# Performance work log

Hardware: AMD Instinct MI355X
Metric: run time of the kernel (lower is better)

Reference implementation:

```python
import jax, jax.numpy as jnp
import numpy as np

B, S, R, C_M = 1, 512, 256, 256   # batch, n_seq, n_res, msa channels
C_P, C_Z = 32, 128                # projection channels, pair channels


def setup_inputs() -> dict:
    key = jax.random.key(0)
    ks = jax.random.split(key, 8)
    M = jax.random.normal(ks[0], (B, S, R, C_M), dtype=jnp.float32)
    M_mask = jnp.ones((B, S, R), dtype=jnp.float32)
    Z_raw = jnp.zeros((B, R, R, C_Z), dtype=jnp.float32)
    # LayerNorm params
    ln_g = jnp.ones((C_M,), dtype=jnp.float32)
    ln_b = jnp.zeros((C_M,), dtype=jnp.float32)
    # linear_a / linear_b: glorot-uniform init
    lim = float(np.sqrt(6.0 / (C_M + C_P)))
    Wa = jax.random.uniform(ks[1], (C_P, C_M), minval=-lim, maxval=lim, dtype=jnp.float32)
    ba = jnp.zeros((C_P,), dtype=jnp.float32)
    Wb = jax.random.uniform(ks[2], (C_P, C_M), minval=-lim, maxval=lim, dtype=jnp.float32)
    bb = jnp.zeros((C_P,), dtype=jnp.float32)
    # o_linear is zero-initialized in the source; use small random weights so the
    # output is non-trivial for correctness testing (math is identical).
    Wo = jax.random.normal(ks[3], (C_Z, C_P * C_P), dtype=jnp.float32) * 0.02
    bo = jnp.zeros((C_Z,), dtype=jnp.float32)
    return {"M": M, "M_mask": M_mask, "Z_raw": Z_raw, "ln_g": ln_g, "ln_b": ln_b,
            "Wa": Wa, "ba": ba, "Wb": Wb, "bb": bb, "Wo": Wo, "bo": bo}


def _layernorm(x, g, b, eps=1e-5):
    mu = jnp.mean(x, axis=-1, keepdims=True)
    var = jnp.var(x, axis=-1, keepdims=True)
    return (x - mu) * jax.lax.rsqrt(var + eps) * g + b


def reference(M, M_mask, Z_raw, ln_g, ln_b, Wa, ba, Wb, bb, Wo, bo):
    Mn = _layernorm(M, ln_g, ln_b)                      # [b,s,i,c_m]
    mask = M_mask[..., None]                            # [b,s,i,1]
    left = (jnp.einsum('bsic,dc->bsid', Mn, Wa) + ba) * mask   # [b,s,i,d]
    right = (jnp.einsum('bsic,ec->bsie', Mn, Wb) + bb) * mask  # [b,s,j,e]
    # outer-product mean: contract over sequence dim s
    O = jnp.einsum('bsid,bsje->bijde', left, right)     # [b,i,j,d,e]
    b, i, j, d, e = O.shape
    O = O.reshape(b, i, j, d * e)
    Z = jnp.einsum('bijk,zk->bijz', O, Wo) + bo         # [b,i,j,c_z]
    norm = jnp.einsum('bsi,bsj->bij', M_mask, M_mask)[..., None]
    return Z / (1e-3 + norm)
```

## Files before the change

### kernel.cpp

```cpp
#include <hip/hip_runtime.h>
#include <hip/hip_bf16.h>
#include <stdint.h>

#define S_DIM 512
#define R_DIM 256
#define CM 256
#define CP 32
#define CZ 128

typedef __attribute__((ext_vector_type(8))) short bf16x8;
typedef __attribute__((ext_vector_type(4))) float f32x4;
typedef unsigned int u32;

__device__ __forceinline__ float bf2f(unsigned short u) {
  union { u32 i; float f; } v; v.i = ((u32)u) << 16; return v.f;
}
__device__ __forceinline__ unsigned short f2bf(float f) {
  union { float f; u32 i; } v; v.f = f;
  u32 x = v.i;
  u32 r = (x + 0x7FFFu + ((x >> 16) & 1u)) >> 16;
  return (unsigned short)r;
}

__device__ __forceinline__ void gload_lds16(const unsigned short* g, unsigned short* l) {
  __builtin_amdgcn_global_load_lds((const __attribute__((address_space(1))) u32*)(g),
                                   (__attribute__((address_space(3))) u32*)(l), 16, 0, 0);
}

__device__ __forceinline__ void wave_bar() {
  asm volatile("" ::: "memory");
  __builtin_amdgcn_s_barrier();
  asm volatile("" ::: "memory");
}

__global__ void prep_kernel(const float* __restrict__ Wa, const float* __restrict__ ba,
                            const float* __restrict__ Wb, const float* __restrict__ bb,
                            const float* __restrict__ ln_g, const float* __restrict__ ln_b,
                            unsigned short* __restrict__ wp, float* __restrict__ Ka,
                            float* __restrict__ Ca) {
  __shared__ float ska[4], sca[4];
  const int o = blockIdx.x;
  const int c = threadIdx.x;
  const float* W = (o < 32) ? (Wa + o * CM) : (Wb + (o - 32) * CM);
  float wv = W[c];
  unsigned short bv = f2bf(wv * ln_g[c]);
  wp[o * CM + c] = bv;
  float ka = bf2f(bv);
  float ca = wv * ln_b[c];
  #pragma unroll
  for (int m = 1; m < 64; m <<= 1) {
    ka += __shfl_xor(ka, m);
    ca += __shfl_xor(ca, m);
  }
  if ((c & 63) == 0) { ska[c >> 6] = ka; sca[c >> 6] = ca; }
  __syncthreads();
  if (c == 0) {
    Ka[o] = ska[0] + ska[1] + ska[2] + ska[3];
    Ca[o] = sca[0] + sca[1] + sca[2] + sca[3] + ((o < 32) ? ba[o] : bb[o - 32]);
  }
}

__global__ void cast_wo_kernel(const float* __restrict__ Wo, unsigned short* __restrict__ Wo_bf) {
  int idx = blockIdx.x * blockDim.x + threadIdx.x;
  if (idx < CZ * CP * CP) Wo_bf[idx] = f2bf(Wo[idx]);
}

__global__ void scale_kernel(const float* __restrict__ mask, float* __restrict__ scale) {
  int i = blockIdx.x, j = threadIdx.x;
  float sum = 0.f;
  for (int s = 0; s < S_DIM; ++s) {
    sum += mask[s * R_DIM + i] * mask[s * R_DIM + j];
  }
  scale[i * R_DIM + j] = 1.0f / (1e-3f + sum);
}

#define K1_ROWS 64
#define XPAD 264

__global__ __launch_bounds__(256) void
ln_proj_kernel(const float* __restrict__ M, const float* __restrict__ mask,
               const unsigned short* __restrict__ wp_g, const float* __restrict__ Ka_g,
               const float* __restrict__ Ca_g,
               unsigned short* __restrict__ leftT, unsigned short* __restrict__ rightT) {
  __shared__ unsigned short xt[K1_ROWS * XPAD];
  __shared__ unsigned short wp[64 * XPAD];
  __shared__ float smu[K1_ROWS], srs[K1_ROWS], smk[K1_ROWS];
  __shared__ float sKa[64], sCa[64];

  const int t = threadIdx.x;
  const int lane = t & 63;
  const int w = t >> 6;
  const int lm = lane & 15;
  const int rr = lane >> 4;
  const int i = blockIdx.x;
  const int s0 = blockIdx.y * K1_ROWS;

  for (int idx = t; idx < 64 * CM / 8; idx += 256) {
    int row = idx >> 5;
    int col = (idx & 31) * 8;
    *(uint4*)(&wp[row * XPAD + col]) = *(const uint4*)(wp_g + row * CM + col);
  }
  if (t < 64) { sKa[t] = Ka_g[t]; sCa[t] = Ca_g[t]; }

  #pragma unroll
  for (int it = 0; it < 4; ++it) {
    const int row = w * 16 + it * 4 + rr;
    const int sg = s0 + row;
    const float* src = M + ((size_t)sg * R_DIM + i) * CM;
    float4 x[4];
    #pragma unroll
    for (int ch = 0; ch < 4; ++ch) x[ch] = *(const float4*)(src + ch * 64 + lm * 4);
    float sum = 0.f, ssq = 0.f;
    #pragma unroll
    for (int ch = 0; ch < 4; ++ch) {
      sum += x[ch].x + x[ch].y + x[ch].z + x[ch].w;
      ssq += x[ch].x * x[ch].x + x[ch].y * x[ch].y + x[ch].z * x[ch].z + x[ch].w * x[ch].w;
    }
    #pragma unroll
    for (int m = 1; m < 16; m <<= 1) {
      sum += __shfl_xor(sum, m);
      ssq += __shfl_xor(ssq, m);
    }
    float mu = sum * (1.0f / CM);
    float var = ssq * (1.0f / CM) - mu * mu;
    float rs = rsqrtf(var + 1e-5f);
    if (lm == 0) {
      smu[row] = mu; srs[row] = rs;
      smk[row] = mask[(size_t)sg * R_DIM + i];
    }
    #pragma unroll
    for (int ch = 0; ch < 4; ++ch) {
      ushort4 xb;
      xb.x = f2bf(x[ch].x); xb.y = f2bf(x[ch].y); xb.z = f2bf(x[ch].z); xb.w = f2bf(x[ch].w);
      *(ushort4*)(&xt[row * XPAD + ch * 64 + lm * 4]) = xb;
    }
  }
  __syncthreads();

  f32x4 acc[4] = {{0.f, 0.f, 0.f, 0.f}, {0.f, 0.f, 0.f, 0.f},
                  {0.f, 0.f, 0.f, 0.f}, {0.f, 0.f, 0.f, 0.f}};
  #pragma unroll
  for (int k = 0; k < 8; ++k) {
    const int c0 = k * 32 + ((lane >> 4) << 3);
    bf16x8 a = *(const bf16x8*)(&wp[(w * 16 + (lane & 15)) * XPAD + c0]);
    #pragma unroll
    for (int nt = 0; nt < 4; ++nt) {
      bf16x8 b = *(const bf16x8*)(&xt[(nt * 16 + (lane & 15)) * XPAD + c0]);
      acc[nt] = __builtin_amdgcn_mfma_f32_16x16x32_bf16(a, b, acc[nt], 0, 0, 0);
    }
  }

  #pragma unroll
  for (int nt = 0; nt < 4; ++nt) {
    int srow = nt * 16 + (lane & 15);
    float mu = smu[srow], rs = srs[srow], mk = smk[srow];
    int sg = s0 + srow;
    #pragma unroll
    for (int r = 0; r < 4; ++r) {
      int o = w * 16 + ((lane >> 4) << 2) + r;
      float v = (rs * (acc[nt][r] - mu * sKa[o]) + sCa[o]) * mk;
      unsigned short bv = f2bf(v);
      if (o < 32) leftT[(size_t)(i * 32 + o) * S_DIM + sg] = bv;
      else        rightT[(size_t)(i * 32 + (o - 32)) * S_DIM + sg] = bv;
    }
  }
}

#define NT2 8

__global__ __launch_bounds__(512, 1) void
opm_gemm_kernel(const unsigned short* __restrict__ leftT, const unsigned short* __restrict__ rightT,
                const unsigned short* __restrict__ Wo_bf, const float* __restrict__ bo,
                const float* __restrict__ scale, float* __restrict__ out) {
  extern __shared__ unsigned short smem[];

  const int t = threadIdx.x;
  const int lane = t & 63;
  const int lm = lane & 15, lq = lane >> 4;
  const int sw = lm & 7;
  const int w = t >> 6;
  const int wm = w >> 2, wn = w & 3;

  const int bid = blockIdx.x;
  const int xcd = bid & 7, local = bid >> 3;
  const int by = xcd * 4 + (local & 3);
  const int bx = local >> 2;

  const unsigned short* Asrc = leftT + (size_t)(by * 256) * S_DIM;
  const unsigned short* Bsrc = rightT + (size_t)(bx * 256) * S_DIM;

  int sr[4], so[4];
  #pragma unroll
  for (int q = 0; q < 4; ++q) {
    int c = q * 512 + t;
    sr[q] = c >> 3;
    so[q] = ((c & 7) ^ ((c >> 3) & 7)) * 8;
  }

  f32x4 acc[8][4];
  #pragma unroll
  for (int a = 0; a < 8; ++a)
    #pragma unroll
    for (int b = 0; b < 4; ++b) acc[a][b] = (f32x4){0.f, 0.f, 0.f, 0.f};

  auto STAGE = [&](int kt, int buf) {
    const int kb = kt * 64;
    unsigned short* ab = smem + buf * 32768;
    #pragma unroll
    for (int q = 0; q < 4; ++q) {
      int c = q * 512 + t;
      gload_lds16(Asrc + (size_t)sr[q] * S_DIM + kb + so[q], ab + c * 8);
      gload_lds16(Bsrc + (size_t)sr[q] * S_DIM + kb + so[q], ab + 16384 + c * 8);
    }
  };

  STAGE(0, 0);
  STAGE(1, 1);

  #pragma unroll
  for (int kt = 0; kt < NT2; ++kt) {
    const int cur = kt & 1;
    if (kt < NT2 - 1) asm volatile("s_waitcnt vmcnt(8)" ::: "memory");
    else              asm volatile("s_waitcnt vmcnt(0)" ::: "memory");
    wave_bar();

    const unsigned short* Ab = smem + cur * 32768;
    const unsigned short* Bb = Ab + 16384;
    #pragma unroll
    for (int ks = 0; ks < 2; ++ks) {
      const int kp = ks * 4 + lq;
      const int slot = (kp ^ sw) << 3;
      bf16x8 af[8], bfr[4];
      #pragma unroll
      for (int mi = 0; mi < 8; ++mi)
        af[mi] = *(const bf16x8*)(&Ab[(wm * 128 + mi * 16 + lm) * 64 + slot]);
      #pragma unroll
      for (int ni = 0; ni < 4; ++ni)
        bfr[ni] = *(const bf16x8*)(&Bb[(wn * 64 + ni * 16 + lm) * 64 + slot]);
      #pragma unroll
      for (int mi = 0; mi < 8; ++mi)
        #pragma unroll
        for (int ni = 0; ni < 4; ++ni)
          acc[mi][ni] = __builtin_amdgcn_mfma_f32_16x16x32_bf16(af[mi], bfr[ni], acc[mi][ni], 0, 0, 0);
    }

    wave_bar();
    if (kt + 2 < NT2) STAGE(kt + 2, cur);
  }

  #pragma unroll
  for (int mi = 0; mi < 8; ++mi) {
    #pragma unroll
    for (int ni = 0; ni < 4; ++ni) {
      const int n = wn * 64 + ni * 16 + lm;
      const int jl = n >> 5, e = n & 31;
      #pragma unroll
      for (int r = 0; r < 4; ++r) {
        const int m = wm * 128 + mi * 16 + lq * 4 + r;
        const int il = m >> 5, d = m & 31;
        const int pair = il * 8 + jl;
        u32 byte = (u32)pair * 2048 + ((((u32)(d * 32 + e)) * 2) ^ ((u32)(pair & 7) << 4));
        *(unsigned short*)((char*)smem + byte) = f2bf(acc[mi][ni][r]);
      }
    }
  }
  __syncthreads();

  f32x4 zacc[4] = {{0.f, 0.f, 0.f, 0.f}, {0.f, 0.f, 0.f, 0.f},
                   {0.f, 0.f, 0.f, 0.f}, {0.f, 0.f, 0.f, 0.f}};
  const unsigned short* wsrc = Wo_bf + (size_t)(w * 16 + lm) * (CP * CP) + lq * 8;
  #pragma unroll 4
  for (int kk = 0; kk < 32; ++kk) {
    bf16x8 bw = *(const bf16x8*)(wsrc + kk * 32);
    #pragma unroll
    for (int pt = 0; pt < 4; ++pt) {
      const int pairL = pt * 16 + lm;
      u32 byte = (u32)pairL * 2048 + (((u32)(kk * 64 + lq * 16)) ^ ((u32)(pairL & 7) << 4));
      bf16x8 a = *(const bf16x8*)((const char*)smem + byte);
      zacc[pt] = __builtin_amdgcn_mfma_f32_16x16x32_bf16(a, bw, zacc[pt], 0, 0, 0);
    }
  }

  const int z = w * 16 + lm;
  const float bz = bo[z];
  #pragma unroll
  for (int pt = 0; pt < 4; ++pt) {
    #pragma unroll
    for (int r = 0; r < 4; ++r) {
      const int pair = pt * 16 + lq * 4 + r;
      const int ig = by * 8 + (pair >> 3), jg = bx * 8 + (pair & 7);
      float v = (zacc[pt][r] + bz) * scale[ig * R_DIM + jg];
      out[((size_t)ig * R_DIM + jg) * CZ + z] = v;
    }
  }
}

extern "C" void kernel_launch(void* const* d_in, const int* in_sizes, int n_in,
                              void* d_out, int out_size, void* d_ws, size_t ws_size,
                              hipStream_t stream) {
  const float* M     = (const float*)d_in[0];
  const float* Mmask = (const float*)d_in[1];
  const float* ln_g  = (const float*)d_in[3];
  const float* ln_b  = (const float*)d_in[4];
  const float* Wa    = (const float*)d_in[5];
  const float* ba    = (const float*)d_in[6];
  const float* Wb    = (const float*)d_in[7];
  const float* bb    = (const float*)d_in[8];
  const float* Wo    = (const float*)d_in[9];
  const float* bo    = (const float*)d_in[10];
  float* out = (float*)d_out;

  char* ws = (char*)d_ws;
  unsigned short* leftT  = (unsigned short*)(ws);
  unsigned short* rightT = (unsigned short*)(ws + 8388608);
  unsigned short* wp     = (unsigned short*)(ws + 16777216);
  float*          Ka     = (float*)(ws + 16810240);
  float*          Ca     = (float*)(ws + 16810496);
  unsigned short* Wo_bf  = (unsigned short*)(ws + 16810752);
  float*          scale  = (float*)(ws + 17072896);
  (void)ws_size; (void)in_sizes; (void)n_in; (void)out_size;

  hipFuncSetAttribute((const void*)opm_gemm_kernel,
                      hipFuncAttributeMaxDynamicSharedMemorySize, 131072);

  hipLaunchKernelGGL(prep_kernel, dim3(64), dim3(256), 0, stream,
                     Wa, ba, Wb, bb, ln_g, ln_b, wp, Ka, Ca);
  hipLaunchKernelGGL(cast_wo_kernel, dim3(512), dim3(256), 0, stream, Wo, Wo_bf);
  hipLaunchKernelGGL(scale_kernel, dim3(R_DIM), dim3(R_DIM), 0, stream, Mmask, scale);
  hipLaunchKernelGGL(ln_proj_kernel, dim3(R_DIM, S_DIM / K1_ROWS), dim3(256), 0, stream,
                     M, Mmask, wp, Ka, Ca, leftT, rightT);
  hipLaunchKernelGGL(opm_gemm_kernel, dim3(1024), dim3(512), 131072, stream,
                     leftT, rightT, Wo_bf, bo, scale, out);
}
```

Measured before the change: 167.0 us.

## Fuse prep kernels and double GEMM workgroup to 16 waves with vectorized epilogue

Merges the three small setup kernels into one launch to cut launch overhead. The main outer-product GEMM now runs with 1024 threads (16 waves), each wave owning a 64x64 tile instead of 128x64. This lowers register pressure per wave and raises the number of waves resident per CU. It also adds s_setprio around the MFMA loop, packs bf16 stores to LDS four at a time using a new transposed Wo layout and swizzle, and splits the second GEMM across wave halves. The risks are more barrier traffic with 16 waves and a more intricate swizzle that must stay consistent between the store and the load side.

```diff
diff --git a/kernel.cpp b/kernel.cpp
--- a/kernel.cpp
+++ b/kernel.cpp
@@ -33,45 +33,48 @@
   asm volatile("" ::: "memory");
 }
 
-__global__ void prep_kernel(const float* __restrict__ Wa, const float* __restrict__ ba,
-                            const float* __restrict__ Wb, const float* __restrict__ bb,
-                            const float* __restrict__ ln_g, const float* __restrict__ ln_b,
-                            unsigned short* __restrict__ wp, float* __restrict__ Ka,
-                            float* __restrict__ Ca) {
-  __shared__ float ska[4], sca[4];
-  const int o = blockIdx.x;
-  const int c = threadIdx.x;
-  const float* W = (o < 32) ? (Wa + o * CM) : (Wb + (o - 32) * CM);
-  float wv = W[c];
-  unsigned short bv = f2bf(wv * ln_g[c]);
-  wp[o * CM + c] = bv;
-  float ka = bf2f(bv);
-  float ca = wv * ln_b[c];
-  #pragma unroll
-  for (int m = 1; m < 64; m <<= 1) {
-    ka += __shfl_xor(ka, m);
-    ca += __shfl_xor(ca, m);
-  }
-  if ((c & 63) == 0) { ska[c >> 6] = ka; sca[c >> 6] = ca; }
-  __syncthreads();
-  if (c == 0) {
-    Ka[o] = ska[0] + ska[1] + ska[2] + ska[3];
-    Ca[o] = sca[0] + sca[1] + sca[2] + sca[3] + ((o < 32) ? ba[o] : bb[o - 32]);
-  }
-}
-
-__global__ void cast_wo_kernel(const float* __restrict__ Wo, unsigned short* __restrict__ Wo_bf) {
-  int idx = blockIdx.x * blockDim.x + threadIdx.x;
-  if (idx < CZ * CP * CP) Wo_bf[idx] = f2bf(Wo[idx]);
-}
-
-__global__ void scale_kernel(const float* __restrict__ mask, float* __restrict__ scale) {
-  int i = blockIdx.x, j = threadIdx.x;
-  float sum = 0.f;
-  for (int s = 0; s < S_DIM; ++s) {
-    sum += mask[s * R_DIM + i] * mask[s * R_DIM + j];
-  }
-  scale[i * R_DIM + j] = 1.0f / (1e-3f + sum);
+__global__ __launch_bounds__(256) void
+fused_prep_kernel(const float* __restrict__ Wa, const float* __restrict__ ba,
+                  const float* __restrict__ Wb, const float* __restrict__ bb,
+                  const float* __restrict__ ln_g, const float* __restrict__ ln_b,
+                  const float* __restrict__ Wo, const float* __restrict__ mask,
+                  unsigned short* __restrict__ wp, float* __restrict__ Ka,
+                  float* __restrict__ Ca, unsigned short* __restrict__ Wo_bf,
+                  float* __restrict__ scale) {
+  const int b = blockIdx.x;
+  const int t = threadIdx.x;
+  if (b < 64) {
+    __shared__ float ska[4], sca[4];
+    const int o = b;
+    const float* W = (o < 32) ? (Wa + o * CM) : (Wb + (o - 32) * CM);
+    float wv = W[t];
+    unsigned short bv = f2bf(wv * ln_g[t]);
+    wp[o * CM + t] = bv;
+    float ka = bf2f(bv);
+    float ca = wv * ln_b[t];
+    #pragma unroll
+    for (int m = 1; m < 64; m <<= 1) {
+      ka += __shfl_xor(ka, m);
+      ca += __shfl_xor(ca, m);
+    }
+    if ((t & 63) == 0) { ska[t >> 6] = ka; sca[t >> 6] = ca; }
+    __syncthreads();
+    if (t == 0) {
+      Ka[o] = ska[0] + ska[1] + ska[2] + ska[3];
+      Ca[o] = sca[0] + sca[1] + sca[2] + sca[3] + ((o < 32) ? ba[o] : bb[o - 32]);
+    }
+  } else if (b < 576) {
+    int idx = (b - 64) * 256 + t;
+    int z = idx >> 10, k = idx & 1023;
+    int d = k >> 5, e = k & 31;
+    Wo_bf[(z << 10) + e * 32 + d] = f2bf(Wo[idx]);
+  } else {
+    const int i = b - 576, j = t;
+    float sum = 0.f;
+    for (int s = 0; s < S_DIM; ++s)
+      sum += mask[s * R_DIM + i] * mask[s * R_DIM + j];
+    scale[i * R_DIM + j] = 1.0f / (1e-3f + sum);
+  }
 }
 
 #define K1_ROWS 64
@@ -168,7 +171,7 @@
 
 #define NT2 8
 
-__global__ __launch_bounds__(512, 1) void
+__global__ __launch_bounds__(1024) void
 opm_gemm_kernel(const unsigned short* __restrict__ leftT, const unsigned short* __restrict__ rightT,
                 const unsigned short* __restrict__ Wo_bf, const float* __restrict__ bo,
                 const float* __restrict__ scale, float* __restrict__ out) {
@@ -179,7 +182,7 @@
   const int lm = lane & 15, lq = lane >> 4;
   const int sw = lm & 7;
   const int w = t >> 6;
-  const int wm = w >> 2, wn = w & 3;
+  const int wmm = w >> 2, wnn = w & 3;
 
   const int bid = blockIdx.x;
   const int xcd = bid & 7, local = bid >> 3;
@@ -189,17 +192,17 @@
   const unsigned short* Asrc = leftT + (size_t)(by * 256) * S_DIM;
   const unsigned short* Bsrc = rightT + (size_t)(bx * 256) * S_DIM;
 
-  int sr[4], so[4];
-  #pragma unroll
-  for (int q = 0; q < 4; ++q) {
-    int c = q * 512 + t;
+  int sr[2], so[2];
+  #pragma unroll
+  for (int q = 0; q < 2; ++q) {
+    int c = q * 1024 + t;
     sr[q] = c >> 3;
     so[q] = ((c & 7) ^ ((c >> 3) & 7)) * 8;
   }
 
-  f32x4 acc[8][4];
-  #pragma unroll
-  for (int a = 0; a < 8; ++a)
+  f32x4 acc[4][4];
+  #pragma unroll
+  for (int a = 0; a < 4; ++a)
     #pragma unroll
     for (int b = 0; b < 4; ++b) acc[a][b] = (f32x4){0.f, 0.f, 0.f, 0.f};
 
@@ -207,8 +210,8 @@
     const int kb = kt * 64;
     unsigned short* ab = smem + buf * 32768;
     #pragma unroll
-    for (int q = 0; q < 4; ++q) {
-      int c = q * 512 + t;
+    for (int q = 0; q < 2; ++q) {
+      int c = q * 1024 + t;
       gload_lds16(Asrc + (size_t)sr[q] * S_DIM + kb + so[q], ab + c * 8);
       gload_lds16(Bsrc + (size_t)sr[q] * S_DIM + kb + so[q], ab + 16384 + c * 8);
     }
@@ -220,7 +223,7 @@
   #pragma unroll
   for (int kt = 0; kt < NT2; ++kt) {
     const int cur = kt & 1;
-    if (kt < NT2 - 1) asm volatile("s_waitcnt vmcnt(8)" ::: "memory");
+    if (kt < NT2 - 1) asm volatile("s_waitcnt vmcnt(4)" ::: "memory");
     else              asm volatile("s_waitcnt vmcnt(0)" ::: "memory");
     wave_bar();
 
@@ -230,18 +233,20 @@
     for (int ks = 0; ks < 2; ++ks) {
       const int kp = ks * 4 + lq;
       const int slot = (kp ^ sw) << 3;
-      bf16x8 af[8], bfr[4];
+      bf16x8 af[4], bfr[4];
       #pragma unroll
-      for (int mi = 0; mi < 8; ++mi)
-        af[mi] = *(const bf16x8*)(&Ab[(wm * 128 + mi * 16 + lm) * 64 + slot]);
+      for (int mi = 0; mi < 4; ++mi)
+        af[mi] = *(const bf16x8*)(&Ab[(wmm * 64 + mi * 16 + lm) * 64 + slot]);
       #pragma unroll
       for (int ni = 0; ni < 4; ++ni)
-        bfr[ni] = *(const bf16x8*)(&Bb[(wn * 64 + ni * 16 + lm) * 64 + slot]);
+        bfr[ni] = *(const bf16x8*)(&Bb[(wnn * 64 + ni * 16 + lm) * 64 + slot]);
+      __builtin_amdgcn_s_setprio(1);
       #pragma unroll
-      for (int mi = 0; mi < 8; ++mi)
+      for (int mi = 0; mi < 4; ++mi)
         #pragma unroll
         for (int ni = 0; ni < 4; ++ni)
           acc[mi][ni] = __builtin_amdgcn_mfma_f32_16x16x32_bf16(af[mi], bfr[ni], acc[mi][ni], 0, 0, 0);
+      __builtin_amdgcn_s_setprio(0);
     }
 
     wave_bar();
@@ -249,45 +254,45 @@
   }
 
   #pragma unroll
-  for (int mi = 0; mi < 8; ++mi) {
+  for (int mi = 0; mi < 4; ++mi) {
+    const int m0 = wmm * 64 + mi * 16 + lq * 4;
+    const int il = m0 >> 5, d0 = m0 & 31;
     #pragma unroll
     for (int ni = 0; ni < 4; ++ni) {
-      const int n = wn * 64 + ni * 16 + lm;
+      const int n = wnn * 64 + ni * 16 + lm;
       const int jl = n >> 5, e = n & 31;
-      #pragma unroll
-      for (int r = 0; r < 4; ++r) {
-        const int m = wm * 128 + mi * 16 + lq * 4 + r;
-        const int il = m >> 5, d = m & 31;
-        const int pair = il * 8 + jl;
-        u32 byte = (u32)pair * 2048 + ((((u32)(d * 32 + e)) * 2) ^ ((u32)(pair & 7) << 4));
-        *(unsigned short*)((char*)smem + byte) = f2bf(acc[mi][ni][r]);
-      }
+      const int pair = il * 8 + jl;
+      u32 off = ((u32)(64 * e + 2 * d0)) ^ ((u32)(e & 7) << 4) ^ ((u32)(pair & 7) << 4);
+      ushort4 v4;
+      v4.x = f2bf(acc[mi][ni][0]); v4.y = f2bf(acc[mi][ni][1]);
+      v4.z = f2bf(acc[mi][ni][2]); v4.w = f2bf(acc[mi][ni][3]);
+      *(ushort4*)((char*)smem + (u32)pair * 2048 + off) = v4;
     }
   }
   __syncthreads();
 
-  f32x4 zacc[4] = {{0.f, 0.f, 0.f, 0.f}, {0.f, 0.f, 0.f, 0.f},
-                   {0.f, 0.f, 0.f, 0.f}, {0.f, 0.f, 0.f, 0.f}};
-  const unsigned short* wsrc = Wo_bf + (size_t)(w * 16 + lm) * (CP * CP) + lq * 8;
-  #pragma unroll 4
+  const int wz = w & 7, wph = w >> 3;
+  f32x4 zacc[2] = {{0.f, 0.f, 0.f, 0.f}, {0.f, 0.f, 0.f, 0.f}};
+  const unsigned short* wsrc = Wo_bf + (size_t)(wz * 16 + lm) * (CP * CP) + lq * 8;
+  #pragma unroll 8
   for (int kk = 0; kk < 32; ++kk) {
     bf16x8 bw = *(const bf16x8*)(wsrc + kk * 32);
     #pragma unroll
-    for (int pt = 0; pt < 4; ++pt) {
-      const int pairL = pt * 16 + lm;
-      u32 byte = (u32)pairL * 2048 + (((u32)(kk * 64 + lq * 16)) ^ ((u32)(pairL & 7) << 4));
-      bf16x8 a = *(const bf16x8*)((const char*)smem + byte);
+    for (int pt = 0; pt < 2; ++pt) {
+      const int pairL = wph * 32 + pt * 16 + lm;
+      u32 off = ((u32)(kk * 64 + lq * 16)) ^ ((u32)(kk & 7) << 4) ^ ((u32)(pairL & 7) << 4);
+      bf16x8 a = *(const bf16x8*)((const char*)smem + (u32)pairL * 2048 + off);
       zacc[pt] = __builtin_amdgcn_mfma_f32_16x16x32_bf16(a, bw, zacc[pt], 0, 0, 0);
     }
   }
 
-  const int z = w * 16 + lm;
+  const int z = wz * 16 + lm;
   const float bz = bo[z];
   #pragma unroll
-  for (int pt = 0; pt < 4; ++pt) {
+  for (int pt = 0; pt < 2; ++pt) {
     #pragma unroll
     for (int r = 0; r < 4; ++r) {
-      const int pair = pt * 16 + lq * 4 + r;
+      const int pair = wph * 32 + pt * 16 + lq * 4 + r;
       const int ig = by * 8 + (pair >> 3), jg = bx * 8 + (pair & 7);
       float v = (zacc[pt][r] + bz) * scale[ig * R_DIM + jg];
       out[((size_t)ig * R_DIM + jg) * CZ + z] = v;
@@ -323,12 +328,10 @@
   hipFuncSetAttribute((const void*)opm_gemm_kernel,
                       hipFuncAttributeMaxDynamicSharedMemorySize, 131072);
 
-  hipLaunchKernelGGL(prep_kernel, dim3(64), dim3(256), 0, stream,
-                     Wa, ba, Wb, bb, ln_g, ln_b, wp, Ka, Ca);
-  hipLaunchKernelGGL(cast_wo_kernel, dim3(512), dim3(256), 0, stream, Wo, Wo_bf);
-  hipLaunchKernelGGL(scale_kernel, dim3(R_DIM), dim3(R_DIM), 0, stream, Mmask, scale);
+  hipLaunchKernelGGL(fused_prep_kernel, dim3(832), dim3(256), 0, stream,
+                     Wa, ba, Wb, bb, ln_g, ln_b, Wo, Mmask, wp, Ka, Ca, Wo_bf, scale);
   hipLaunchKernelGGL(ln_proj_kernel, dim3(R_DIM, S_DIM / K1_ROWS), dim3(256), 0, stream,
                      M, Mmask, wp, Ka, Ca, leftT, rightT);
-  hipLaunchKernelGGL(opm_gemm_kernel, dim3(1024), dim3(512), 131072, stream,
+  hipLaunchKernelGGL(opm_gemm_kernel, dim3(1024), dim3(1024), 131072, stream,
                      leftT, rightT, Wo_bf, bo, scale, out);
 }
```

Result: slower. 184.7 us (+10.6%).
